# Kernel tuning notes

Measured on AMD Instinct MI355X. Metric: run time of the kernel, lower is better.

The kernel has to match this reference:

```python
import jax, jax.numpy as jnp
import numpy as np

HIDDEN_DIM = 1024
SEQ_LEN = 4096
D_IN = 1024


def setup_inputs() -> dict:
    key = jax.random.key(0)
    ks = jax.random.split(key, 9)
    s = 1.0 / np.sqrt(D_IN)
    return {
        "q": jax.random.normal(ks[0], (SEQ_LEN, D_IN), jnp.float32),
        "k": jax.random.normal(ks[1], (SEQ_LEN, D_IN), jnp.float32),
        "v": jax.random.normal(ks[2], (SEQ_LEN, D_IN), jnp.float32),
        "Wq": jax.random.normal(ks[3], (D_IN, HIDDEN_DIM), jnp.float32) * s,
        "bq": jnp.zeros((HIDDEN_DIM,), jnp.float32),
        "Wk": jax.random.normal(ks[4], (D_IN, HIDDEN_DIM), jnp.float32) * s,
        "bk": jnp.zeros((HIDDEN_DIM,), jnp.float32),
        "Wv": jax.random.normal(ks[5], (D_IN, HIDDEN_DIM), jnp.float32) * s,
        "bv": jnpp_zeros() if False else jnp.zeros((HIDDEN_DIM,), jnp.float32),
    }


def reference(q, k, v, Wq, bq, Wk, bk, Wv, bv):
    # Dense projections (flax Dense: x @ W + b)
    query = q @ Wq + bq          # [S, H]
    key_p = k @ Wk + bk          # [S, H]
    value = v @ Wv + bv          # [S, H]
    # scores = Q K^T / sqrt(hidden_dim)  -> [S, S]
    scores = jnp.matmul(query, key_p.T) / jnp.sqrt(jnp.float32(HIDDEN_DIM))
    weights = jax.nn.softmax(scores, axis=-1)
    context = jnp.matmul(weights, value)  # [S, H]
    return context
```

## Files before the change

kernel.cpp:

```cpp
#include <hip/hip_runtime.h>


typedef short short4v __attribute__((ext_vector_type(4)));
typedef short short8  __attribute__((ext_vector_type(8)));
typedef float f32x4   __attribute__((ext_vector_type(4)));

#define MFMA16 __builtin_amdgcn_mfma_f32_16x16x32_bf16

__device__ __forceinline__ short f2bf(float f) {
    union { float f; unsigned u; } x; x.f = f;
    unsigned r = (x.u + 0x7FFFu + ((x.u >> 16) & 1u)) >> 16;
    return (short)r;
}
__device__ __forceinline__ float bf2f(short s) {
    union { unsigned u; float f; } x;
    x.u = ((unsigned)(unsigned short)s) << 16; return x.f;
}
__device__ __forceinline__ void store_out(short* p, float v) { *p = f2bf(v); }
__device__ __forceinline__ void store_out(float* p, float v) { *p = v; }

__device__ __forceinline__ void gl2lds(const short* g, short* l) {
    __builtin_amdgcn_global_load_lds(
        (const __attribute__((address_space(1))) void*)g,
        (__attribute__((address_space(3))) void*)l, 16, 0, 0);
}

__global__ __launch_bounds__(256) void prep_w(
    const float* __restrict__ W0, const float* __restrict__ W1,
    const float* __restrict__ W2, short* __restrict__ Wt)
{
    __shared__ float tile[64][65];
    const float* W = blockIdx.z == 0 ? W0 : (blockIdx.z == 1 ? W1 : W2);
    short* T = Wt + (size_t)blockIdx.z * 1048576;
    const int c0 = blockIdx.x * 64;
    const int r0 = blockIdx.y * 64;
    const int tx = threadIdx.x & 63;
    const int ty = threadIdx.x >> 6;
    #pragma unroll
    for (int p = 0; p < 16; ++p) {
        int r = ty + p * 4;
        tile[r][tx] = W[(size_t)(r0 + r) * 1024 + c0 + tx];
    }
    __syncthreads();
    #pragma unroll
    for (int p = 0; p < 16; ++p) {
        int r = ty + p * 4;
        T[(size_t)(c0 + r) * 1024 + r0 + tx] = f2bf(tile[tx][r]);
    }
}

__global__ __launch_bounds__(256) void cast_qkv(
    const float* __restrict__ q, const float* __restrict__ k,
    const float* __restrict__ v, short* __restrict__ xb)
{
    const float* src = blockIdx.z == 0 ? q : (blockIdx.z == 1 ? k : v);
    short* dst = xb + (size_t)blockIdx.z * 4194304;
    for (int i = blockIdx.x * 256 + threadIdx.x; i < 1048576; i += 256 * 1024) {
        float4 f = ((const float4*)src)[i];
        short4v o;
        o[0] = f2bf(f.x); o[1] = f2bf(f.y); o[2] = f2bf(f.z); o[3] = f2bf(f.w);
        ((short4v*)dst)[i] = o;
    }
}

template <typename TOut, int MODE>
__global__ __launch_bounds__(256) void gemm64(
    const short* __restrict__ A, const short* __restrict__ Bt,
    const float* __restrict__ b0, const float* __restrict__ b1,
    const float* __restrict__ b2, TOut* __restrict__ C,
    short* __restrict__ Vt,
    int M, int N, int Kd, int lda, int ldb, float scale, int kiters)
{
    constexpr int LDSN = (MODE == 1) ? (128 * 136) : (128 * 64 * 2);
    __shared__ short Lds[LDSN];
    short* As = Lds;
    short* Bs = Lds + 128 * 64;

    const int t    = threadIdx.x;
    const int lane = t & 63;
    const int wv   = t >> 6;

    const int nb  = gridDim.x;
    const int bid = blockIdx.y * nb + blockIdx.x;
    const int band   = bid / (8 * nb);
    const int within = bid - band * 8 * nb;
    const int m0 = (band * 8 + (within & 7)) * 128;
    const int n0 = (within >> 3) * 128;

    const float* bias = nullptr;
    int kbeg = 0;
    if constexpr (MODE == 1) {
        const int z = blockIdx.z;
        A  += (size_t)z * M * lda;
        Bt += (size_t)z * N * ldb;
        C  += (size_t)z * M * N;
        bias = z == 0 ? b0 : (z == 1 ? b1 : b2);
    }
    if constexpr (MODE == 2) {
        kbeg = blockIdx.z * kiters * 64;
        C += (size_t)blockIdx.z * M * N;
    }
    (void)b0; (void)b1; (void)b2;

    const int sr = lane >> 3;
    const int sc = (lane & 7) ^ sr;
    const short* pA = A  + (size_t)(m0 + wv * 32 + sr) * lda + kbeg + sc * 8;
    const short* pB = Bt + (size_t)(n0 + wv * 32 + sr) * ldb + kbeg + sc * 8;
    const size_t a8 = (size_t)8 * lda;
    const size_t b8 = (size_t)8 * ldb;
    short* lA = As + wv * 2048;
    short* lB = Bs + wv * 2048;

    const int wm = wv & 1, wn = wv >> 1;
    const int lr = lane & 15, lq = lane >> 4;
    const int xkey = lr & 7;

    f32x4 acc[4][4];
    #pragma unroll
    for (int i = 0; i < 4; ++i)
        #pragma unroll
        for (int j = 0; j < 4; ++j) {
            f32x4 z = {0.f, 0.f, 0.f, 0.f};
            acc[i][j] = z;
        }

    for (int kk = 0; kk < kiters; ++kk) {
        #pragma unroll
        for (int r = 0; r < 4; ++r) gl2lds(pA + r * a8, lA + r * 512);
        #pragma unroll
        for (int r = 0; r < 4; ++r) gl2lds(pB + r * b8, lB + r * 512);
        pA += 64; pB += 64;
        __syncthreads();

        #pragma unroll
        for (int h = 0; h < 2; ++h) {
            short8 af[4], bfr[4];
            #pragma unroll
            for (int i = 0; i < 4; ++i)
                af[i] = *(const short8*)
                    &As[(wm * 64 + i * 16 + lr) * 64 + (((h * 4 + lq) ^ xkey) * 8)];
            #pragma unroll
            for (int j = 0; j < 4; ++j)
                bfr[j] = *(const short8*)
                    &Bs[(wn * 64 + j * 16 + lr) * 64 + (((h * 4 + lq) ^ xkey) * 8)];
            #pragma unroll
            for (int i = 0; i < 4; ++i)
                #pragma unroll
                for (int j = 0; j < 4; ++j)
                    acc[i][j] = MFMA16(af[i], bfr[j], acc[i][j], 0, 0, 0);
        }
        __syncthreads();
    }

    if constexpr (MODE == 1) {
        if (blockIdx.z == 2) {
            #pragma unroll
            for (int i = 0; i < 4; ++i) {
                #pragma unroll
                for (int j = 0; j < 4; ++j) {
                    const int colL = wn * 64 + j * 16 + lr;
                    const float bb = bias[n0 + colL];
                    #pragma unroll
                    for (int r = 0; r < 4; ++r) {
                        const int rowL = wm * 64 + i * 16 + lq * 4 + r;
                        Lds[colL * 136 + rowL] = f2bf(acc[i][j][r] * scale + bb);
                    }
                }
            }
            __syncthreads();
            const int c = t >> 1, part = t & 1;
            short* dst = Vt + (size_t)(n0 + c) * 4096 + m0 + part * 64;
            #pragma unroll
            for (int s = 0; s < 8; ++s)
                *(short8*)(dst + s * 8) =
                    *(const short8*)&Lds[c * 136 + part * 64 + s * 8];
            return;
        }
    }
    #pragma unroll
    for (int i = 0; i < 4; ++i) {
        #pragma unroll
        for (int j = 0; j < 4; ++j) {
            const int crow = m0 + wm * 64 + i * 16 + lq * 4;
            const int ccol = n0 + wn * 64 + j * 16 + lr;
            float bb = 0.f;
            if constexpr (MODE == 1) bb = bias[ccol];
            #pragma unroll
            for (int r = 0; r < 4; ++r) {
                float val = acc[i][j][r] * scale + bb;
                store_out(&C[(size_t)(crow + r) * N + ccol], val);
            }
        }
    }
}

__global__ __launch_bounds__(256) void softmax_bf16(short* __restrict__ S)
{
    const int row = blockIdx.x;
    short8* r8 = (short8*)(S + (size_t)row * 4096);
    const int t = threadIdx.x;

    float x[16];
    #pragma unroll
    for (int i = 0; i < 2; ++i) {
        short8 raw = r8[t + 256 * i];
        #pragma unroll
        for (int j = 0; j < 8; ++j) x[8 * i + j] = bf2f(raw[j]);
    }
    float m = -1e30f;
    #pragma unroll
    for (int i = 0; i < 16; ++i) m = fmaxf(m, x[i]);
    #pragma unroll
    for (int off = 32; off > 0; off >>= 1) m = fmaxf(m, __shfl_xor(m, off));

    __shared__ float redm[4], reds[4];
    const int wv = t >> 6;
    if ((t & 63) == 0) redm[wv] = m;
    __syncthreads();
    m = fmaxf(fmaxf(redm[0], redm[1]), fmaxf(redm[2], redm[3]));

    float s = 0.f;
    #pragma unroll
    for (int i = 0; i < 16; ++i) { x[i] = __expf(x[i] - m); s += x[i]; }
    #pragma unroll
    for (int off = 32; off > 0; off >>= 1) s += __shfl_xor(s, off);
    if ((t & 63) == 0) reds[wv] = s;
    __syncthreads();
    s = reds[0] + reds[1] + reds[2] + reds[3];
    const float inv = 1.f / s;

    #pragma unroll
    for (int i = 0; i < 2; ++i) {
        short8 o;
        #pragma unroll
        for (int j = 0; j < 8; ++j) o[j] = f2bf(x[8 * i + j] * inv);
        r8[t + 256 * i] = o;
    }
}

__global__ __launch_bounds__(256) void combine(
    const float* __restrict__ p0, const float* __restrict__ p1,
    float* __restrict__ out)
{
    for (int i = blockIdx.x * 256 + threadIdx.x; i < 1048576; i += 256 * 1024) {
        float4 a = ((const float4*)p0)[i];
        float4 b = ((const float4*)p1)[i];
        float4 o; o.x = a.x + b.x; o.y = a.y + b.y;
        o.z = a.z + b.z; o.w = a.w + b.w;
        ((float4*)out)[i] = o;
    }
}

extern "C" void kernel_launch(void* const* d_in, const int* in_sizes, int n_in,
                              void* d_out, int out_size, void* d_ws, size_t ws_size,
                              hipStream_t stream)
{
    const float* q  = (const float*)d_in[0];
    const float* k  = (const float*)d_in[1];
    const float* v  = (const float*)d_in[2];
    const float* Wq = (const float*)d_in[3];
    const float* bq = (const float*)d_in[4];
    const float* Wk = (const float*)d_in[5];
    const float* bk = (const float*)d_in[6];
    const float* Wv = (const float*)d_in[7];
    const float* bv = (const float*)d_in[8];
    float* out = (float*)d_out;

    char* ws = (char*)d_ws;
    const size_t MB = 1ull << 20;
    short* Wt = (short*)(ws + 0);
    short* xb = (short*)(ws + 6 * MB);
    short* pr = (short*)(ws + 30 * MB);
    short* Vt = (short*)(ws + 46 * MB);
    short* S  = (short*)(ws + 54 * MB);
    float* p0 = (float*)(ws + 0);
    float* p1 = p0 + 4194304;

    prep_w<<<dim3(16, 16, 3), 256, 0, stream>>>(Wq, Wk, Wv, Wt);
    cast_qkv<<<dim3(1024, 1, 3), 256, 0, stream>>>(q, k, v, xb);
    gemm64<short, 1><<<dim3(8, 32, 3), 256, 0, stream>>>(
        xb, Wt, bq, bk, bv, pr, Vt, 4096, 1024, 1024, 1024, 1024, 1.f, 16);
    gemm64<short, 0><<<dim3(32, 32), 256, 0, stream>>>(
        pr, pr + 4194304, nullptr, nullptr, nullptr, S, nullptr,
        4096, 4096, 1024, 1024, 1024, 0.03125f, 16);
    softmax_bf16<<<4096, 256, 0, stream>>>(S);
    gemm64<float, 2><<<dim3(8, 32, 2), 256, 0, stream>>>(
        S, Vt, nullptr, nullptr, nullptr, p0, nullptr,
        4096, 1024, 4096, 4096, 4096, 1.f, 32);
    combine<<<1024, 256, 0, stream>>>(p0, p1, out);
}
```

Baseline: 268.0 us.

## Switch GEMMs to 32x32x16 MFMA and split final GEMM three ways

Replaces the 16x16x32 bf16 MFMA tiling with 32x32x16 MFMA (2x2 accumulators per wave), which halves the LDS fragment loads per K step and issues fewer, larger matrix instructions. The epilogue row mapping is rewritten for the 32x32 output layout. The P·V GEMM goes from split-K 2 to split-K 3 for more blocks, with the last split writing directly into the output. The combine kernel then adds the other two partials into it in place. This adds one more partial buffer and a read-modify-write of the output.

```diff
diff --git a/kernel.cpp b/kernel.cpp
--- a/kernel.cpp
+++ b/kernel.cpp
@@ -3,9 +3,9 @@
 
 typedef short short4v __attribute__((ext_vector_type(4)));
 typedef short short8  __attribute__((ext_vector_type(8)));
-typedef float f32x4   __attribute__((ext_vector_type(4)));
-
-#define MFMA16 __builtin_amdgcn_mfma_f32_16x16x32_bf16
+typedef float f32x16  __attribute__((ext_vector_type(16)));
+
+#define MFMA32 __builtin_amdgcn_mfma_f32_32x32x16_bf16
 
 __device__ __forceinline__ short f2bf(float f) {
     union { float f; unsigned u; } x; x.f = f;
@@ -63,12 +63,12 @@
     }
 }
 
-template <typename TOut, int MODE>
-__global__ __launch_bounds__(256) void gemm64(
+template <typename TOut, int MODE, int SK = 1>
+__global__ __launch_bounds__(256) void gemm_mfma(
     const short* __restrict__ A, const short* __restrict__ Bt,
     const float* __restrict__ b0, const float* __restrict__ b1,
     const float* __restrict__ b2, TOut* __restrict__ C,
-    short* __restrict__ Vt,
+    float* __restrict__ Cout, short* __restrict__ Vt,
     int M, int N, int Kd, int lda, int ldb, float scale, int kiters)
 {
     constexpr int LDSN = (MODE == 1) ? (128 * 136) : (128 * 64 * 2);
@@ -89,6 +89,8 @@
 
     const float* bias = nullptr;
     int kbeg = 0;
+    int myk  = kiters;
+    float* Cw = nullptr;
     if constexpr (MODE == 1) {
         const int z = blockIdx.z;
         A  += (size_t)z * M * lda;
@@ -97,10 +99,16 @@
         bias = z == 0 ? b0 : (z == 1 ? b1 : b2);
     }
     if constexpr (MODE == 2) {
-        kbeg = blockIdx.z * kiters * 64;
-        C += (size_t)blockIdx.z * M * N;
-    }
-    (void)b0; (void)b1; (void)b2;
+        const int z = blockIdx.z;
+        kbeg = z * kiters * 64;
+        if (z == SK - 1) {
+            myk = (Kd >> 6) - (SK - 1) * kiters;
+            Cw  = Cout;
+        } else {
+            Cw = (float*)C + (size_t)z * M * N;
+        }
+    }
+    (void)b0; (void)b1; (void)b2; (void)Cout;
 
     const int sr = lane >> 3;
     const int sc = (lane & 7) ^ sr;
@@ -112,19 +120,18 @@
     short* lB = Bs + wv * 2048;
 
     const int wm = wv & 1, wn = wv >> 1;
-    const int lr = lane & 15, lq = lane >> 4;
-    const int xkey = lr & 7;
-
-    f32x4 acc[4][4];
-    #pragma unroll
-    for (int i = 0; i < 4; ++i)
-        #pragma unroll
-        for (int j = 0; j < 4; ++j) {
-            f32x4 z = {0.f, 0.f, 0.f, 0.f};
-            acc[i][j] = z;
-        }
-
-    for (int kk = 0; kk < kiters; ++kk) {
+    const int cl = lane & 31;
+    const int g  = lane >> 5;
+    const int xk = lane & 7;
+
+    f32x16 acc[2][2];
+    #pragma unroll
+    for (int i = 0; i < 2; ++i)
+        #pragma unroll
+        for (int j = 0; j < 2; ++j)
+            acc[i][j] = (f32x16)(0.f);
+
+    for (int kk = 0; kk < myk; ++kk) {
         #pragma unroll
         for (int r = 0; r < 4; ++r) gl2lds(pA + r * a8, lA + r * 512);
         #pragma unroll
@@ -133,21 +140,20 @@
         __syncthreads();
 
         #pragma unroll
-        for (int h = 0; h < 2; ++h) {
-            short8 af[4], bfr[4];
-            #pragma unroll
-            for (int i = 0; i < 4; ++i)
-                af[i] = *(const short8*)
-                    &As[(wm * 64 + i * 16 + lr) * 64 + (((h * 4 + lq) ^ xkey) * 8)];
-            #pragma unroll
-            for (int j = 0; j < 4; ++j)
-                bfr[j] = *(const short8*)
-                    &Bs[(wn * 64 + j * 16 + lr) * 64 + (((h * 4 + lq) ^ xkey) * 8)];
-            #pragma unroll
-            for (int i = 0; i < 4; ++i)
+        for (int ks = 0; ks < 4; ++ks) {
+            const int chunk = ((ks * 2 + g) ^ xk) * 8;
+            short8 af[2], bfr[2];
+            #pragma unroll
+            for (int i = 0; i < 2; ++i)
+                af[i] = *(const short8*)&As[(wm * 64 + i * 32 + cl) * 64 + chunk];
+            #pragma unroll
+            for (int j = 0; j < 2; ++j)
+                bfr[j] = *(const short8*)&Bs[(wn * 64 + j * 32 + cl) * 64 + chunk];
+            #pragma unroll
+            for (int i = 0; i < 2; ++i)
                 #pragma unroll
-                for (int j = 0; j < 4; ++j)
-                    acc[i][j] = MFMA16(af[i], bfr[j], acc[i][j], 0, 0, 0);
+                for (int j = 0; j < 2; ++j)
+                    acc[i][j] = MFMA32(af[i], bfr[j], acc[i][j], 0, 0, 0);
         }
         __syncthreads();
     }
@@ -155,14 +161,14 @@
     if constexpr (MODE == 1) {
         if (blockIdx.z == 2) {
             #pragma unroll
-            for (int i = 0; i < 4; ++i) {
+            for (int i = 0; i < 2; ++i) {
                 #pragma unroll
-                for (int j = 0; j < 4; ++j) {
-                    const int colL = wn * 64 + j * 16 + lr;
+                for (int j = 0; j < 2; ++j) {
+                    const int colL = wn * 64 + j * 32 + cl;
                     const float bb = bias[n0 + colL];
                     #pragma unroll
-                    for (int r = 0; r < 4; ++r) {
-                        const int rowL = wm * 64 + i * 16 + lq * 4 + r;
+                    for (int r = 0; r < 16; ++r) {
+                        const int rowL = wm * 64 + i * 32 + (r & 3) + 8 * (r >> 2) + 4 * g;
                         Lds[colL * 136 + rowL] = f2bf(acc[i][j][r] * scale + bb);
                     }
                 }
@@ -178,17 +184,20 @@
         }
     }
     #pragma unroll
-    for (int i = 0; i < 4; ++i) {
-        #pragma unroll
-        for (int j = 0; j < 4; ++j) {
-            const int crow = m0 + wm * 64 + i * 16 + lq * 4;
-            const int ccol = n0 + wn * 64 + j * 16 + lr;
+    for (int i = 0; i < 2; ++i) {
+        #pragma unroll
+        for (int j = 0; j < 2; ++j) {
+            const int ccol = n0 + wn * 64 + j * 32 + cl;
             float bb = 0.f;
             if constexpr (MODE == 1) bb = bias[ccol];
             #pragma unroll
-            for (int r = 0; r < 4; ++r) {
-                float val = acc[i][j][r] * scale + bb;
-                store_out(&C[(size_t)(crow + r) * N + ccol], val);
+            for (int r = 0; r < 16; ++r) {
+                const int crow = m0 + wm * 64 + i * 32 + (r & 3) + 8 * (r >> 2) + 4 * g;
+                const float val = acc[i][j][r] * scale + bb;
+                if constexpr (MODE == 2)
+                    Cw[(size_t)crow * N + ccol] = val;
+                else
+                    store_out(&C[(size_t)crow * N + ccol], val);
             }
         }
     }
@@ -238,15 +247,16 @@
     }
 }
 
-__global__ __launch_bounds__(256) void combine(
+__global__ __launch_bounds__(256) void combine3(
     const float* __restrict__ p0, const float* __restrict__ p1,
     float* __restrict__ out)
 {
     for (int i = blockIdx.x * 256 + threadIdx.x; i < 1048576; i += 256 * 1024) {
         float4 a = ((const float4*)p0)[i];
         float4 b = ((const float4*)p1)[i];
-        float4 o; o.x = a.x + b.x; o.y = a.y + b.y;
-        o.z = a.z + b.z; o.w = a.w + b.w;
+        float4 o = ((const float4*)out)[i];
+        o.x += a.x + b.x; o.y += a.y + b.y;
+        o.z += a.z + b.z; o.w += a.w + b.w;
         ((float4*)out)[i] = o;
     }
 }
@@ -273,19 +283,19 @@
     short* pr = (short*)(ws + 30 * MB);
     short* Vt = (short*)(ws + 46 * MB);
     short* S  = (short*)(ws + 54 * MB);
-    float* p0 = (float*)(ws + 0);
-    float* p1 = p0 + 4194304;
+    float* pp = (float*)(ws + 0);
 
     prep_w<<<dim3(16, 16, 3), 256, 0, stream>>>(Wq, Wk, Wv, Wt);
     cast_qkv<<<dim3(1024, 1, 3), 256, 0, stream>>>(q, k, v, xb);
-    gemm64<short, 1><<<dim3(8, 32, 3), 256, 0, stream>>>(
-        xb, Wt, bq, bk, bv, pr, Vt, 4096, 1024, 1024, 1024, 1024, 1.f, 16);
-    gemm64<short, 0><<<dim3(32, 32), 256, 0, stream>>>(
-        pr, pr + 4194304, nullptr, nullptr, nullptr, S, nullptr,
+    gemm_mfma<short, 1><<<dim3(8, 32, 3), 256, 0, stream>>>(
+        xb, Wt, bq, bk, bv, pr, nullptr, Vt,
+        4096, 1024, 1024, 1024, 1024, 1.f, 16);
+    gemm_mfma<short, 0><<<dim3(32, 32), 256, 0, stream>>>(
+        pr, pr + 4194304, nullptr, nullptr, nullptr, S, nullptr, nullptr,
         4096, 4096, 1024, 1024, 1024, 0.03125f, 16);
     softmax_bf16<<<4096, 256, 0, stream>>>(S);
-    gemm64<float, 2><<<dim3(8, 32, 2), 256, 0, stream>>>(
-        S, Vt, nullptr, nullptr, nullptr, p0, nullptr,
-        4096, 1024, 4096, 4096, 4096, 1.f, 32);
-    combine<<<1024, 256, 0, stream>>>(p0, p1, out);
-}
+    gemm_mfma<float, 2, 3><<<dim3(8, 32, 3), 256, 0, stream>>>(
+        S, Vt, nullptr, nullptr, nullptr, pp, out, nullptr,
+        4096, 1024, 4096, 4096, 4096, 1.f, 21);
+    combine3<<<1024, 256, 0, stream>>>(pp, pp + 4194304, out);
+}
```

Result: no change. 271.1 us (+1.1%).
